# Kernel optimization log

Hardware: AMD Instinct MI355X
Metric: run time of the kernel (lower is better)

Reference implementation:

```python
import jax, jax.numpy as jnp
import numpy as np

H = 32          # num_heads
D = 64          # head_dim
HID = 2048      # hidden_size
THETA = 10000.0
GATE_NORM = 16.0
EPS = 1e-6


def rope_interleaved(x):
    # x: [B, T, H, D]; interleaved RoPE over full head_dim, 'fla' inv_freq
    B, T, nh, d = x.shape
    inv_freq = 1.0 / (THETA ** (jnp.arange(0, d, 2, dtype=jnp.float32) / d))  # [d/2]
    t = jnp.arange(T, dtype=jnp.float32)
    freqs = t[:, None] * inv_freq[None, :]                 # [T, d/2]
    cos = jnp.cos(freqs)[None, :, None, :]                 # [1,T,1,d/2]
    sin = jnp.sin(freqs)[None, :, None, :]
    x1 = x[..., 0::2]
    x2 = x[..., 1::2]
    r1 = x1 * cos - x2 * sin
    r2 = x1 * sin + x2 * cos
    out = jnp.stack([r1, r2], axis=-1).reshape(x.shape)    # re-interleave pairs
    return out


def setup_inputs() -> dict:
    key = jax.random.key(0)
    ks = jax.random.split(key, 7)
    s = HID ** -0.5
    return {
        "hidden_states": jax.random.normal(ks[0], (1, 2048, HID), dtype=jnp.float32),
        "Wq": jax.random.normal(ks[1], (HID, HID), dtype=jnp.float32) * s,
        "Wk": jax.random.normal(ks[2], (HID, HID), dtype=jnp.float32) * s,
        "Wv": jax.random.normal(ks[3], (HID, HID), dtype=jnp.float32) * s,
        "Wg": jax.random.normal(ks[4], (HID, HID), dtype=jnp.float32) * s,
        "Wgk": jax.random.normal(ks[5], (H, HID), dtype=jnp.float32) * s,
        "Wo": jax.random.normal(ks[6], (HID, HID), dtype=jnp.float32) * s,
    }


def reference(hidden_states, Wq, Wk, Wv, Wg, Wgk, Wo):
    B, T, _ = hidden_states.shape
    q = (hidden_states @ Wq.T).reshape(B, T, H, D)
    k = (hidden_states @ Wk.T).reshape(B, T, H, D)
    v = (hidden_states @ Wv.T).reshape(B, T, H, D)
    g = hidden_states @ Wg.T                                   # [B,T,HID]
    gk = jax.nn.log_sigmoid(hidden_states @ Wgk.T) / GATE_NORM  # [B,T,H], <= 0

    q = rope_interleaved(q)
    k = rope_interleaved(k)

    # gated retention (simple GLA) in parallel form:
    # o_t = scale * sum_{s<=t} exp(G_t - G_s) (q_t . k_s) v_s,  G = cumsum(gk)
    scale = D ** -0.5
    G = jnp.cumsum(gk, axis=1)                                 # [B,T,H]
    Gt = jnp.transpose(G, (0, 2, 1))                           # [B,H,T]
    decay = Gt[:, :, :, None] - Gt[:, :, None, :]              # [B,H,T,T] (<=0 on causal part)
    causal = jnp.tril(jnp.ones((T, T), dtype=bool))
    scores = jnp.einsum('bihd,bjhd->bhij', q, k) * scale
    A = jnp.where(causal[None, None], jnp.exp(decay) * scores, 0.0)
    o = jnp.einsum('bhij,bjhd->bihd', A, v)                    # [B,T,H,D]

    # FusedRMSNormGated (no affine): rmsnorm(o) * silu(gate)
    var = jnp.mean(jnp.square(o), axis=-1, keepdims=True)
    o = o * jax.lax.rsqrt(var + EPS)
    gate = g.reshape(B, T, H, D)
    o = o * jax.nn.silu(gate)

    o = o.reshape(B, T, HID) @ Wo.T
    return o
```

## Files before the change

### kernel.cpp

```cpp
#include <hip/hip_runtime.h>
#include <hip/hip_bf16.h>
#include <stdint.h>

#define TT 2048
#define NH 32
#define HD 64
#define HIDDEN 2048

typedef __attribute__((ext_vector_type(8))) short short8;
typedef __attribute__((ext_vector_type(4))) short short4v;
typedef __attribute__((ext_vector_type(4))) float f32x4;

__device__ inline short f2bf(float x) {
  __hip_bfloat16 h = __float2bfloat16(x);
  return __builtin_bit_cast(short, h);
}

__device__ inline void gload16(const void* g, void* l) {
  __builtin_amdgcn_global_load_lds(
      (const __attribute__((address_space(1))) unsigned int*)g,
      (__attribute__((address_space(3))) unsigned int*)l, 16, 0, 0);
}

__global__ void cast6(const float* __restrict__ s0, const float* __restrict__ s1,
                      const float* __restrict__ s2, const float* __restrict__ s3,
                      const float* __restrict__ s4, const float* __restrict__ s5,
                      short* __restrict__ d0, short* __restrict__ d1,
                      short* __restrict__ d2, short* __restrict__ d3,
                      short* __restrict__ d4, short* __restrict__ d5) {
  int t0 = blockIdx.x * 256 + threadIdx.x;
  int stride = gridDim.x * 256;
  const int NG = 1 << 20;
#define CAST_LOOP(S, D)                                            \
  for (int g = t0; g < NG; g += stride) {                          \
    float4 v = *reinterpret_cast<const float4*>(S + (size_t)g * 4);\
    short4v o;                                                     \
    o[0] = f2bf(v.x); o[1] = f2bf(v.y);                            \
    o[2] = f2bf(v.z); o[3] = f2bf(v.w);                            \
    *reinterpret_cast<short4v*>(D + (size_t)g * 4) = o;            \
  }
  CAST_LOOP(s0, d0)
  CAST_LOOP(s1, d1)
  CAST_LOOP(s2, d2)
  CAST_LOOP(s3, d3)
  CAST_LOOP(s4, d4)
  CAST_LOOP(s5, d5)
#undef CAST_LOOP
}

__global__ void rope_table_kernel(float2* __restrict__ rt) {
  int idx = blockIdx.x * 256 + threadIdx.x;
  int t = idx >> 5, i = idx & 31;
  float inv = exp2f(-(float)i * (13.287712379549449f / 32.0f));
  float f = (float)t * inv;
  float2 cs; cs.x = cosf(f); cs.y = sinf(f);
  rt[idx] = cs;
}

__global__ __launch_bounds__(256) void gk_kernel(const float* __restrict__ hidden,
                                                 const float* __restrict__ Wgk,
                                                 float* __restrict__ gk) {
  int t = blockIdx.x;
  __shared__ float row[HIDDEN];
  int tid = threadIdx.x;
  const float4* hr = reinterpret_cast<const float4*>(hidden + (size_t)t * HIDDEN);
#pragma unroll
  for (int i = 0; i < 2; i++) {
    float4 v = hr[tid + i * 256];
    *reinterpret_cast<float4*>(&row[(tid + i * 256) * 4]) = v;
  }
  __syncthreads();
  int w = tid >> 6, l = tid & 63;
  for (int hh = 0; hh < 8; hh++) {
    int h = w * 8 + hh;
    const float* wr = Wgk + (size_t)h * HIDDEN;
    float acc = 0.f;
#pragma unroll
    for (int i = 0; i < 32; i++) acc = fmaf(row[i * 64 + l], wr[i * 64 + l], acc);
#pragma unroll
    for (int m = 1; m < 64; m <<= 1) acc += __shfl_xor(acc, m, 64);
    if (l == 0) {
      float x = acc;
      float ls = fminf(x, 0.f) - log1pf(__expf(-fabsf(x)));
      gk[(size_t)h * TT + t] = ls * (1.0f / 16.0f);
    }
  }
}

__global__ void cumsum_kernel(const float* __restrict__ gk, float* __restrict__ G) {
  int h = blockIdx.x;
  int l = threadIdx.x;
  float carry = 0.f;
  for (int c = 0; c < 32; c++) {
    float x = gk[(size_t)h * TT + c * 64 + l];
#pragma unroll
    for (int ofs = 1; ofs < 64; ofs <<= 1) {
      float y = __shfl_up(x, ofs, 64);
      if (l >= ofs) x += y;
    }
    x += carry;
    G[(size_t)h * TT + c * 64 + l] = x;
    carry = __shfl(x, 63, 64);
  }
}

__global__ __launch_bounds__(512, 1) void gemm256(const short* __restrict__ A,
                                                  const short* __restrict__ B,
                                                  float* __restrict__ C,
                                                  int M, int N, int K) {
  __shared__ short lds[4 * 16384];
  int tid = threadIdx.x;
  int w = tid >> 6, l = tid & 63;
  int wr = w >> 2, wc = w & 3;
  int lr = l & 15, lg = l >> 4;

  int bx = blockIdx.x, by = blockIdx.y;
  if ((gridDim.x & 7) == 0) {
    int id = by * gridDim.x + bx;
    int sx = gridDim.x >> 3;
    int xcd = id & 7, p = id >> 3;
    bx = xcd * sx + p % sx;
    by = p / sx;
  }
  size_t tm = (size_t)by * 256, tn = (size_t)bx * 256;

  int srow = l >> 2;
  int schunk = (((l & 3) ^ ((l >> 2) & 3) ^ ((l >> 4) & 3)) << 3);
  const short* pA0 = A + (size_t)(tm + w * 16 + srow) * K + schunk;
  const short* pA1 = A + (size_t)(tm + 128 + w * 16 + srow) * K + schunk;
  const short* pB0 = B + (size_t)(tn + w * 16 + srow) * K + schunk;
  const short* pB1 = B + (size_t)(tn + 128 + w * 16 + srow) * K + schunk;
  int dA0 = (0 * 128 + w * 16) * 32;
  int dA1 = (1 * 128 + w * 16) * 32;
  int dB0 = 8192 + (0 * 128 + w * 16) * 32;
  int dB1 = 8192 + (1 * 128 + w * 16) * 32;

  int rchunk = ((lg ^ ((lr & 3) ^ ((lr >> 2) & 3))) << 3);
  int baseA = (wr * 128 + lr) * 32 + rchunk;
  int baseB = (wc * 64 + lr) * 32 + rchunk;

  f32x4 acc[8][4] = {};
  int nt = K >> 5;

  for (int t = 0; t < 3; ++t) {
    short* sb = &lds[(t & 3) * 16384];
    gload16(pA0 + (size_t)t * 32, sb + dA0);
    gload16(pA1 + (size_t)t * 32, sb + dA1);
    gload16(pB0 + (size_t)t * 32, sb + dB0);
    gload16(pB1 + (size_t)t * 32, sb + dB1);
  }
  asm volatile("s_waitcnt vmcnt(8)" ::: "memory");
  __builtin_amdgcn_s_barrier();

  for (int t = 0; t < nt; ++t) {
    const short* As = &lds[(t & 3) * 16384];
    const short* Bs = As + 8192;
    int pf = t + 3;
    bool do_pf = pf < nt;
    short* pfb = &lds[(pf & 3) * 16384];

    short8 a[4], b[4];
#pragma unroll
    for (int mi = 0; mi < 4; mi++)
      a[mi] = *reinterpret_cast<const short8*>(As + baseA + mi * 512);
#pragma unroll
    for (int ni = 0; ni < 4; ni++)
      b[ni] = *reinterpret_cast<const short8*>(Bs + baseB + ni * 512);
    if (do_pf) {
      gload16(pA0 + (size_t)pf * 32, pfb + dA0);
      gload16(pA1 + (size_t)pf * 32, pfb + dA1);
    }
    __builtin_amdgcn_s_barrier();
    asm volatile("s_waitcnt lgkmcnt(0)" ::: "memory");
    __builtin_amdgcn_s_setprio(1);
#pragma unroll
    for (int mi = 0; mi < 4; mi++)
#pragma unroll
      for (int ni = 0; ni < 4; ni++)
        acc[mi][ni] = __builtin_amdgcn_mfma_f32_16x16x32_bf16(a[mi], b[ni], acc[mi][ni], 0, 0, 0);
    __builtin_amdgcn_s_setprio(0);
    __builtin_amdgcn_s_barrier();

#pragma unroll
    for (int mi = 0; mi < 4; mi++)
      a[mi] = *reinterpret_cast<const short8*>(As + baseA + (mi + 4) * 512);
    if (do_pf) {
      gload16(pB0 + (size_t)pf * 32, pfb + dB0);
      gload16(pB1 + (size_t)pf * 32, pfb + dB1);
    }
    __builtin_amdgcn_s_barrier();
    asm volatile("s_waitcnt lgkmcnt(0)" ::: "memory");
    __builtin_amdgcn_s_setprio(1);
#pragma unroll
    for (int mi = 0; mi < 4; mi++)
#pragma unroll
      for (int ni = 0; ni < 4; ni++)
        acc[mi + 4][ni] = __builtin_amdgcn_mfma_f32_16x16x32_bf16(a[mi], b[ni], acc[mi + 4][ni], 0, 0, 0);
    __builtin_amdgcn_s_setprio(0);
    asm volatile("s_waitcnt vmcnt(8)" ::: "memory");
    __builtin_amdgcn_s_barrier();
  }

#pragma unroll
  for (int mi = 0; mi < 8; mi++)
#pragma unroll
    for (int ni = 0; ni < 4; ni++)
#pragma unroll
      for (int r = 0; r < 4; r++) {
        size_t row = tm + wr * 128 + mi * 16 + lg * 4 + r;
        size_t col = tn + wc * 64 + ni * 16 + lr;
        C[row * N + col] = acc[mi][ni][r];
      }
}

__global__ __launch_bounds__(256) void gemm_bt(const short* __restrict__ A,
                                               const short* __restrict__ B,
                                               float* __restrict__ C,
                                               int M, int N, int K) {
  __shared__ short As[128 * 32];
  __shared__ short Bs[128 * 32];
  int tm = blockIdx.y * 128;
  int tn = blockIdx.x * 128;
  int tid = threadIdx.x;
  int w = tid >> 6, l = tid & 63;
  int wr = w >> 1, wc = w & 1;
  int srow = l >> 2;
  int scol = (l & 3) * 8;
  int lg = l >> 4, lr = l & 15;
  f32x4 acc[4][4] = {};
  for (int k0 = 0; k0 < K; k0 += 32) {
    __syncthreads();
#pragma unroll
    for (int i = 0; i < 2; i++) {
      int r = i * 64 + w * 16 + srow;
      gload16(A + (size_t)(tm + r) * K + k0 + scol, &As[(i * 64 + w * 16) * 32]);
      gload16(B + (size_t)(tn + r) * K + k0 + scol, &Bs[(i * 64 + w * 16) * 32]);
    }
    __syncthreads();
    short8 a[4], b[4];
#pragma unroll
    for (int m = 0; m < 4; m++)
      a[m] = *reinterpret_cast<const short8*>(&As[(wr * 64 + m * 16 + lr) * 32 + lg * 8]);
#pragma unroll
    for (int n = 0; n < 4; n++)
      b[n] = *reinterpret_cast<const short8*>(&Bs[(wc * 64 + n * 16 + lr) * 32 + lg * 8]);
#pragma unroll
    for (int m = 0; m < 4; m++)
#pragma unroll
      for (int n = 0; n < 4; n++)
        acc[m][n] = __builtin_amdgcn_mfma_f32_16x16x32_bf16(a[m], b[n], acc[m][n], 0, 0, 0);
  }
#pragma unroll
  for (int m = 0; m < 4; m++)
#pragma unroll
    for (int n = 0; n < 4; n++)
#pragma unroll
      for (int r = 0; r < 4; r++) {
        int row = tm + wr * 64 + m * 16 + lg * 4 + r;
        int col = tn + wc * 64 + n * 16 + lr;
        C[(size_t)row * N + col] = acc[m][n][r];
      }
}

__global__ __launch_bounds__(256) void rope_post(const float* __restrict__ QKVG,
                                                 const float2* __restrict__ rt,
                                                 short* __restrict__ qb,
                                                 short* __restrict__ kb,
                                                 short* __restrict__ vtb) {
  int tb = blockIdx.x, h = blockIdx.y;
  int tid = threadIdx.x;
  int p = tid & 31;
  int r0 = tid >> 5;
#pragma unroll
  for (int rr = 0; rr < 8; rr++) {
    int rloc = r0 * 8 + rr;
    int t = tb * 64 + rloc;
    float2 cs = rt[(size_t)t * 32 + p];
    float2 xq = *reinterpret_cast<const float2*>(&QKVG[(size_t)t * 8192 + h * 64 + 2 * p]);
    float r1 = xq.x * cs.x - xq.y * cs.y;
    float r2 = xq.x * cs.y + xq.y * cs.x;
    ushort2 uq; uq.x = (unsigned short)f2bf(r1); uq.y = (unsigned short)f2bf(r2);
    *reinterpret_cast<ushort2*>(&qb[((size_t)h * TT + t) * 64 + 2 * p]) = uq;
    float2 xk = *reinterpret_cast<const float2*>(&QKVG[(size_t)t * 8192 + 2048 + h * 64 + 2 * p]);
    r1 = xk.x * cs.x - xk.y * cs.y;
    r2 = xk.x * cs.y + xk.y * cs.x;
    ushort2 uk; uk.x = (unsigned short)f2bf(r1); uk.y = (unsigned short)f2bf(r2);
    *reinterpret_cast<ushort2*>(&kb[((size_t)h * TT + t) * 64 + 2 * p]) = uk;
  }
  __shared__ float vt[64][65];
  int c = tid & 63;
  int rbase = tid >> 6;
#pragma unroll
  for (int k4 = 0; k4 < 16; k4++) {
    int rloc = rbase * 16 + k4;
    vt[rloc][c] = QKVG[(size_t)(tb * 64 + rloc) * 8192 + 4096 + h * 64 + c];
  }
  __syncthreads();
#pragma unroll
  for (int k4 = 0; k4 < 16; k4++) {
    int d = rbase * 16 + k4;
    float val = vt[c][d];
    vtb[((size_t)h * HD + d) * TT + tb * 64 + c] = f2bf(val);
  }
}

__global__ __launch_bounds__(256) void attn_kernel(const short* __restrict__ qbuf,
                                                   const short* __restrict__ kbuf,
                                                   const short* __restrict__ vtbuf,
                                                   const float* __restrict__ G,
                                                   const float* __restrict__ QKVG,
                                                   short* __restrict__ z) {
  int qblk = blockIdx.x, h = blockIdx.y;
  __shared__ short Ks[64 * 64];
  __shared__ short Vs[64 * 64];
  __shared__ short Ps[4][16 * 64];
  int tid = threadIdx.x, w = tid >> 6, l = tid & 63;
  int lg = l >> 4, lr = l & 15;

  int tq_row = qblk * 64 + w * 16 + lr;
  short8 aq0 = *reinterpret_cast<const short8*>(&qbuf[((size_t)h * TT + tq_row) * HD + lg * 8]);
  short8 aq1 = *reinterpret_cast<const short8*>(&qbuf[((size_t)h * TT + tq_row) * HD + 32 + lg * 8]);

  int tq0 = qblk * 64 + w * 16 + lg * 4;
  float Gq[4];
#pragma unroll
  for (int r = 0; r < 4; r++) Gq[r] = G[(size_t)h * TT + tq0 + r];

  f32x4 o[4] = {};
  int sj = w * 8 + (l >> 3);

  for (int jb = 0; jb <= qblk; jb++) {
    __syncthreads();
#pragma unroll
    for (int i = 0; i < 2; i++) {
      int row = i * 32 + sj;
      int cb = ((l & 7) ^ (row & 7)) * 8;
      gload16(&kbuf[((size_t)h * TT + jb * 64 + row) * HD + cb], &Ks[(i * 32 + w * 8) * 64]);
      gload16(&vtbuf[((size_t)h * HD + row) * TT + jb * 64 + cb], &Vs[(i * 32 + w * 8) * 64]);
    }
    __syncthreads();

#pragma unroll
    for (int n = 0; n < 4; n++) {
      int j = n * 16 + lr;
      short8 bk0 = *reinterpret_cast<const short8*>((const char*)Ks + j * 128 + ((lg * 16) ^ ((j & 7) << 4)));
      short8 bk1 = *reinterpret_cast<const short8*>((const char*)Ks + j * 128 + ((64 + lg * 16) ^ ((j & 7) << 4)));
      f32x4 s = {};
      s = __builtin_amdgcn_mfma_f32_16x16x32_bf16(aq0, bk0, s, 0, 0, 0);
      s = __builtin_amdgcn_mfma_f32_16x16x32_bf16(aq1, bk1, s, 0, 0, 0);
      int tj = jb * 64 + n * 16 + lr;
      float Gk = G[(size_t)h * TT + tj];
#pragma unroll
      for (int r = 0; r < 4; r++) {
        int tq = tq0 + r;
        float pv = 0.f;
        if (tj <= tq) pv = __expf(Gq[r] - Gk) * 0.125f * s[r];
        int qloc = lg * 4 + r;
        int jloc = n * 16 + lr;
        int boff = qloc * 128 + ((jloc * 2) ^ ((qloc & 7) << 4));
        *reinterpret_cast<short*>((char*)&Ps[w][0] + boff) = f2bf(pv);
      }
    }

    short8 pa0 = *reinterpret_cast<const short8*>((const char*)&Ps[w][0] + lr * 128 + ((lg * 16) ^ ((lr & 7) << 4)));
    short8 pa1 = *reinterpret_cast<const short8*>((const char*)&Ps[w][0] + lr * 128 + ((64 + lg * 16) ^ ((lr & 7) << 4)));
    __builtin_amdgcn_s_setprio(1);
#pragma unroll
    for (int n = 0; n < 4; n++) {
      int d = n * 16 + lr;
      short8 bv0 = *reinterpret_cast<const short8*>((const char*)Vs + d * 128 + ((lg * 16) ^ ((d & 7) << 4)));
      short8 bv1 = *reinterpret_cast<const short8*>((const char*)Vs + d * 128 + ((64 + lg * 16) ^ ((d & 7) << 4)));
      o[n] = __builtin_amdgcn_mfma_f32_16x16x32_bf16(pa0, bv0, o[n], 0, 0, 0);
      o[n] = __builtin_amdgcn_mfma_f32_16x16x32_bf16(pa1, bv1, o[n], 0, 0, 0);
    }
    __builtin_amdgcn_s_setprio(0);
  }

  float sums[4];
#pragma unroll
  for (int r = 0; r < 4; r++) {
    float ss = 0.f;
#pragma unroll
    for (int n = 0; n < 4; n++) ss += o[n][r] * o[n][r];
#pragma unroll
    for (int m = 1; m < 16; m <<= 1) ss += __shfl_xor(ss, m, 64);
    sums[r] = ss;
  }
#pragma unroll
  for (int r = 0; r < 4; r++) {
    int tq = tq0 + r;
    float rstd = rsqrtf(sums[r] * (1.0f / 64.0f) + 1e-6f);
#pragma unroll
    for (int n = 0; n < 4; n++) {
      int d = n * 16 + lr;
      float gv = QKVG[(size_t)tq * 8192 + 6144 + h * 64 + d];
      float sg = gv / (1.0f + __expf(-gv));
      float val = o[n][r] * rstd * sg;
      z[(size_t)tq * HIDDEN + h * 64 + d] = f2bf(val);
    }
  }
}

extern "C" void kernel_launch(void* const* d_in, const int* in_sizes, int n_in,
                              void* d_out, int out_size, void* d_ws, size_t ws_size,
                              hipStream_t stream) {
  const float* hidden = (const float*)d_in[0];
  const float* Wq = (const float*)d_in[1];
  const float* Wk = (const float*)d_in[2];
  const float* Wv = (const float*)d_in[3];
  const float* Wg = (const float*)d_in[4];
  const float* Wgk = (const float*)d_in[5];
  const float* Wo = (const float*)d_in[6];
  float* out = (float*)d_out;
  char* ws = (char*)d_ws;

  const size_t NELEM = (size_t)TT * HIDDEN;
  short* XbZ  = (short*)(ws + 0);
  short* Wb   = (short*)(ws + 8388608);
  short* Wob  = (short*)(ws + 41943040);
  float* QKVG = (float*)(ws + 50331648);
  short* qbuf = (short*)(ws + 117440512);
  short* kbuf = (short*)(ws + 125829120);
  short* vtbuf= (short*)(ws + 134217728);
  float* gkb  = (float*)(ws + 142606336);
  float* Gb   = (float*)(ws + 142868480);
  float2* rt  = (float2*)(ws + 143130624);

  cast6<<<2048, 256, 0, stream>>>(hidden, Wq, Wk, Wv, Wg, Wo,
                                  XbZ, Wb + 0 * NELEM, Wb + 1 * NELEM,
                                  Wb + 2 * NELEM, Wb + 3 * NELEM, Wob);
  rope_table_kernel<<<256, 256, 0, stream>>>(rt);
  gk_kernel<<<TT, 256, 0, stream>>>(hidden, Wgk, gkb);
  cumsum_kernel<<<NH, 64, 0, stream>>>(gkb, Gb);
  gemm256<<<dim3(32, 8), 512, 0, stream>>>(XbZ, Wb, QKVG, TT, 4 * HIDDEN, HIDDEN);
  rope_post<<<dim3(32, NH), 256, 0, stream>>>(QKVG, rt, qbuf, kbuf, vtbuf);
  attn_kernel<<<dim3(32, NH), 256, 0, stream>>>(qbuf, kbuf, vtbuf, Gb, QKVG, XbZ);
  gemm_bt<<<dim3(16, 16), 256, 0, stream>>>(XbZ, Wob, out, TT, HIDDEN, HIDDEN);
}
```

Measured before the change: 394.5 us.

## Double-buffer K/V tiles and pair causal query blocks per attention workgroup

The attention kernel now double-buffers K and V tiles in LDS, issuing the next tile's async global-to-LDS loads before computing on the current one and waiting with explicit vmcnt counts. Each workgroup also handles two query blocks (bx and 31-bx), so every block does the same total causal work. The grid is halved to 16x32 to match. This aims to hide load latency and remove the causal tail imbalance, at the cost of fewer workgroups (512), more LDS per block, and a reliance on hand-written waitcnt values being correct.

```diff
diff --git a/kernel.cpp b/kernel.cpp
--- a/kernel.cpp
+++ b/kernel.cpp
@@ -310,93 +310,117 @@
                                                    const float* __restrict__ G,
                                                    const float* __restrict__ QKVG,
                                                    short* __restrict__ z) {
-  int qblk = blockIdx.x, h = blockIdx.y;
-  __shared__ short Ks[64 * 64];
-  __shared__ short Vs[64 * 64];
+  int bx = blockIdx.x, h = blockIdx.y;
+  __shared__ short Ks[2][64 * 64];
+  __shared__ short Vs[2][64 * 64];
   __shared__ short Ps[4][16 * 64];
   int tid = threadIdx.x, w = tid >> 6, l = tid & 63;
   int lg = l >> 4, lr = l & 15;
-
-  int tq_row = qblk * 64 + w * 16 + lr;
-  short8 aq0 = *reinterpret_cast<const short8*>(&qbuf[((size_t)h * TT + tq_row) * HD + lg * 8]);
-  short8 aq1 = *reinterpret_cast<const short8*>(&qbuf[((size_t)h * TT + tq_row) * HD + 32 + lg * 8]);
-
-  int tq0 = qblk * 64 + w * 16 + lg * 4;
-  float Gq[4];
-#pragma unroll
-  for (int r = 0; r < 4; r++) Gq[r] = G[(size_t)h * TT + tq0 + r];
-
-  f32x4 o[4] = {};
   int sj = w * 8 + (l >> 3);
-
-  for (int jb = 0; jb <= qblk; jb++) {
-    __syncthreads();
+  const size_t hTT = (size_t)h * TT;
+  const size_t hHD = (size_t)h * HD;
+
+  for (int job = 0; job < 2; job++) {
+    int qblk = job ? 31 - bx : bx;
+
+    int tq_row = qblk * 64 + w * 16 + lr;
+    short8 aq0 = *reinterpret_cast<const short8*>(&qbuf[(hTT + tq_row) * HD + lg * 8]);
+    short8 aq1 = *reinterpret_cast<const short8*>(&qbuf[(hTT + tq_row) * HD + 32 + lg * 8]);
+
+    int tq0 = qblk * 64 + w * 16 + lg * 4;
+    float Gq[4];
+#pragma unroll
+    for (int r = 0; r < 4; r++) Gq[r] = G[hTT + tq0 + r];
+
+    f32x4 o[4] = {};
+
 #pragma unroll
     for (int i = 0; i < 2; i++) {
       int row = i * 32 + sj;
       int cb = ((l & 7) ^ (row & 7)) * 8;
-      gload16(&kbuf[((size_t)h * TT + jb * 64 + row) * HD + cb], &Ks[(i * 32 + w * 8) * 64]);
-      gload16(&vtbuf[((size_t)h * HD + row) * TT + jb * 64 + cb], &Vs[(i * 32 + w * 8) * 64]);
-    }
-    __syncthreads();
-
-#pragma unroll
-    for (int n = 0; n < 4; n++) {
-      int j = n * 16 + lr;
-      short8 bk0 = *reinterpret_cast<const short8*>((const char*)Ks + j * 128 + ((lg * 16) ^ ((j & 7) << 4)));
-      short8 bk1 = *reinterpret_cast<const short8*>((const char*)Ks + j * 128 + ((64 + lg * 16) ^ ((j & 7) << 4)));
-      f32x4 s = {};
-      s = __builtin_amdgcn_mfma_f32_16x16x32_bf16(aq0, bk0, s, 0, 0, 0);
-      s = __builtin_amdgcn_mfma_f32_16x16x32_bf16(aq1, bk1, s, 0, 0, 0);
-      int tj = jb * 64 + n * 16 + lr;
-      float Gk = G[(size_t)h * TT + tj];
-#pragma unroll
-      for (int r = 0; r < 4; r++) {
-        int tq = tq0 + r;
-        float pv = 0.f;
-        if (tj <= tq) pv = __expf(Gq[r] - Gk) * 0.125f * s[r];
-        int qloc = lg * 4 + r;
-        int jloc = n * 16 + lr;
-        int boff = qloc * 128 + ((jloc * 2) ^ ((qloc & 7) << 4));
-        *reinterpret_cast<short*>((char*)&Ps[w][0] + boff) = f2bf(pv);
-      }
-    }
-
-    short8 pa0 = *reinterpret_cast<const short8*>((const char*)&Ps[w][0] + lr * 128 + ((lg * 16) ^ ((lr & 7) << 4)));
-    short8 pa1 = *reinterpret_cast<const short8*>((const char*)&Ps[w][0] + lr * 128 + ((64 + lg * 16) ^ ((lr & 7) << 4)));
-    __builtin_amdgcn_s_setprio(1);
-#pragma unroll
-    for (int n = 0; n < 4; n++) {
-      int d = n * 16 + lr;
-      short8 bv0 = *reinterpret_cast<const short8*>((const char*)Vs + d * 128 + ((lg * 16) ^ ((d & 7) << 4)));
-      short8 bv1 = *reinterpret_cast<const short8*>((const char*)Vs + d * 128 + ((64 + lg * 16) ^ ((d & 7) << 4)));
-      o[n] = __builtin_amdgcn_mfma_f32_16x16x32_bf16(pa0, bv0, o[n], 0, 0, 0);
-      o[n] = __builtin_amdgcn_mfma_f32_16x16x32_bf16(pa1, bv1, o[n], 0, 0, 0);
-    }
-    __builtin_amdgcn_s_setprio(0);
-  }
-
-  float sums[4];
-#pragma unroll
-  for (int r = 0; r < 4; r++) {
-    float ss = 0.f;
-#pragma unroll
-    for (int n = 0; n < 4; n++) ss += o[n][r] * o[n][r];
-#pragma unroll
-    for (int m = 1; m < 16; m <<= 1) ss += __shfl_xor(ss, m, 64);
-    sums[r] = ss;
-  }
-#pragma unroll
-  for (int r = 0; r < 4; r++) {
-    int tq = tq0 + r;
-    float rstd = rsqrtf(sums[r] * (1.0f / 64.0f) + 1e-6f);
-#pragma unroll
-    for (int n = 0; n < 4; n++) {
-      int d = n * 16 + lr;
-      float gv = QKVG[(size_t)tq * 8192 + 6144 + h * 64 + d];
-      float sg = gv / (1.0f + __expf(-gv));
-      float val = o[n][r] * rstd * sg;
-      z[(size_t)tq * HIDDEN + h * 64 + d] = f2bf(val);
+      gload16(&kbuf[(hTT + row) * HD + cb], &Ks[0][(i * 32 + w * 8) * 64]);
+      gload16(&vtbuf[(hHD + row) * TT + cb], &Vs[0][(i * 32 + w * 8) * 64]);
+    }
+
+    for (int jb = 0; jb <= qblk; jb++) {
+      int slot = jb & 1;
+      if (jb < qblk) {
+        int nj = jb + 1, ns = slot ^ 1;
+#pragma unroll
+        for (int i = 0; i < 2; i++) {
+          int row = i * 32 + sj;
+          int cb = ((l & 7) ^ (row & 7)) * 8;
+          gload16(&kbuf[(hTT + (size_t)nj * 64 + row) * HD + cb], &Ks[ns][(i * 32 + w * 8) * 64]);
+          gload16(&vtbuf[(hHD + row) * TT + (size_t)nj * 64 + cb], &Vs[ns][(i * 32 + w * 8) * 64]);
+        }
+        asm volatile("s_waitcnt vmcnt(4)" ::: "memory");
+      } else {
+        asm volatile("s_waitcnt vmcnt(0)" ::: "memory");
+      }
+      __syncthreads();
+
+      const char* Kp = (const char*)&Ks[slot][0];
+      const char* Vp = (const char*)&Vs[slot][0];
+
+#pragma unroll
+      for (int n = 0; n < 4; n++) {
+        int j = n * 16 + lr;
+        short8 bk0 = *reinterpret_cast<const short8*>(Kp + j * 128 + ((lg * 16) ^ ((j & 7) << 4)));
+        short8 bk1 = *reinterpret_cast<const short8*>(Kp + j * 128 + ((64 + lg * 16) ^ ((j & 7) << 4)));
+        f32x4 s = {};
+        s = __builtin_amdgcn_mfma_f32_16x16x32_bf16(aq0, bk0, s, 0, 0, 0);
+        s = __builtin_amdgcn_mfma_f32_16x16x32_bf16(aq1, bk1, s, 0, 0, 0);
+        int tj = jb * 64 + n * 16 + lr;
+        float Gk = G[hTT + tj];
+#pragma unroll
+        for (int r = 0; r < 4; r++) {
+          int tq = tq0 + r;
+          float pv = 0.f;
+          if (tj <= tq) pv = __expf(Gq[r] - Gk) * 0.125f * s[r];
+          int qloc = lg * 4 + r;
+          int jloc = n * 16 + lr;
+          int boff = qloc * 128 + ((jloc * 2) ^ ((qloc & 7) << 4));
+          *reinterpret_cast<short*>((char*)&Ps[w][0] + boff) = f2bf(pv);
+        }
+      }
+
+      short8 pa0 = *reinterpret_cast<const short8*>((const char*)&Ps[w][0] + lr * 128 + ((lg * 16) ^ ((lr & 7) << 4)));
+      short8 pa1 = *reinterpret_cast<const short8*>((const char*)&Ps[w][0] + lr * 128 + ((64 + lg * 16) ^ ((lr & 7) << 4)));
+      __builtin_amdgcn_s_setprio(1);
+#pragma unroll
+      for (int n = 0; n < 4; n++) {
+        int d = n * 16 + lr;
+        short8 bv0 = *reinterpret_cast<const short8*>(Vp + d * 128 + ((lg * 16) ^ ((d & 7) << 4)));
+        short8 bv1 = *reinterpret_cast<const short8*>(Vp + d * 128 + ((64 + lg * 16) ^ ((d & 7) << 4)));
+        o[n] = __builtin_amdgcn_mfma_f32_16x16x32_bf16(pa0, bv0, o[n], 0, 0, 0);
+        o[n] = __builtin_amdgcn_mfma_f32_16x16x32_bf16(pa1, bv1, o[n], 0, 0, 0);
+      }
+      __builtin_amdgcn_s_setprio(0);
+      __syncthreads();
+    }
+
+    float sums[4];
+#pragma unroll
+    for (int r = 0; r < 4; r++) {
+      float ss = 0.f;
+#pragma unroll
+      for (int n = 0; n < 4; n++) ss += o[n][r] * o[n][r];
+#pragma unroll
+      for (int m = 1; m < 16; m <<= 1) ss += __shfl_xor(ss, m, 64);
+      sums[r] = ss;
+    }
+#pragma unroll
+    for (int r = 0; r < 4; r++) {
+      int tq = tq0 + r;
+      float rstd = rsqrtf(sums[r] * (1.0f / 64.0f) + 1e-6f);
+#pragma unroll
+      for (int n = 0; n < 4; n++) {
+        int d = n * 16 + lr;
+        float gv = QKVG[(size_t)tq * 8192 + 6144 + h * 64 + d];
+        float sg = gv / (1.0f + __expf(-gv));
+        float val = o[n][r] * rstd * sg;
+        z[(size_t)tq * HIDDEN + h * 64 + d] = f2bf(val);
+      }
     }
   }
 }
@@ -434,6 +458,6 @@
   cumsum_kernel<<<NH, 64, 0, stream>>>(gkb, Gb);
   gemm256<<<dim3(32, 8), 512, 0, stream>>>(XbZ, Wb, QKVG, TT, 4 * HIDDEN, HIDDEN);
   rope_post<<<dim3(32, NH), 256, 0, stream>>>(QKVG, rt, qbuf, kbuf, vtbuf);
-  attn_kernel<<<dim3(32, NH), 256, 0, stream>>>(qbuf, kbuf, vtbuf, Gb, QKVG, XbZ);
+  attn_kernel<<<dim3(16, NH), 256, 0, stream>>>(qbuf, kbuf, vtbuf, Gb, QKVG, XbZ);
   gemm_bt<<<dim3(16, 16), 256, 0, stream>>>(XbZ, Wob, out, TT, HIDDEN, HIDDEN);
 }
```

Result: no change. 389.0 us (-1.4%).
